# Performance work log

Hardware: AMD Instinct MI355X
Metric: run time of the kernel (lower is better)

## Reference

```python
import jax, jax.numpy as jnp
import numpy as np

MARGIN = 0.1
SCALE_POS = 2.0
SCALE_NEG = 50.0
THRESH = 0.5
EPS = 1e-5


def setup_inputs() -> dict:
    key = jax.random.key(0)
    k1, k2 = jax.random.split(key)
    feats = jax.random.normal(k1, (4096, 2, 192), dtype=jnp.float32)
    labels = jax.random.randint(k2, (4096,), 0, 4096, dtype=jnp.int64)
    return {"feats": feats, "labels": labels}


def reference(feats, labels):
    B, n_utt, D = feats.shape
    lab = jnp.repeat(labels, n_utt)            # [N]
    f = feats.reshape(-1, D)                   # [N, D]
    N = f.shape[0]

    sim = f @ f.T                              # [N, N]
    # F.normalize(sim): L2-normalize each row, eps=1e-12
    row_norm = jnp.maximum(jnp.linalg.norm(sim, axis=1, keepdims=True), 1e-12)
    S = sim / row_norm

    same = lab[None, :] == lab[:, None]        # [N, N]
    pos_mask = same & (S < 1.0 - EPS)          # pos_pair_ (includes self if < 1-eps)
    neg_mask = ~same                           # neg_pair_

    min_pos = jnp.min(jnp.where(pos_mask, S, jnp.inf), axis=1)    # per-row min(pos_pair_)
    max_neg = jnp.max(jnp.where(neg_mask, S, -jnp.inf), axis=1)   # per-row max(neg_pair_)

    neg_keep = neg_mask & (S > (min_pos - MARGIN)[:, None])
    pos_keep = pos_mask & (S < (max_neg + MARGIN)[:, None])

    has_neg = jnp.any(neg_keep, axis=1)
    has_pos = jnp.any(pos_keep, axis=1)
    valid = has_neg & has_pos

    pos_sum = jnp.sum(jnp.where(pos_keep, jnp.exp(-SCALE_POS * (S - THRESH)), 0.0), axis=1)
    neg_sum = jnp.sum(jnp.where(neg_keep, jnp.exp(SCALE_NEG * (S - THRESH)), 0.0), axis=1)

    row_loss = (1.0 / SCALE_POS) * jnp.log1p(pos_sum) + (1.0 / SCALE_NEG) * jnp.log1p(neg_sum)
    loss = jnp.sum(jnp.where(valid, row_loss, 0.0)) / N

    # prec1 = percent of rows skipped for having no surviving negatives
    prec1 = jnp.sum(~has_neg).astype(jnp.float32) * 100.0 / N
    return loss, prec1
```

## Files before the change

kernel.cpp:

```cpp
#include <hip/hip_runtime.h>
#include <math.h>

typedef __bf16 bf16x8 __attribute__((ext_vector_type(8)));
typedef float  f32x4  __attribute__((ext_vector_type(4)));
typedef int    int4v  __attribute__((ext_vector_type(4)));

constexpr float MARGIN    = 0.1f;
constexpr float SCALE_POS = 2.0f;
constexpr float SCALE_NEG = 50.0f;
constexpr float THRESH    = 0.5f;
constexpr float ONE_EPS   = 1.0f - 1e-5f;
constexpr float LOG2E     = 1.4426950408889634f;
constexpr float BC        = -(SCALE_NEG * THRESH * LOG2E);
constexpr float VCUT_COEF = (36.0674f - 30.0f) / (SCALE_NEG * LOG2E);

constexpr int D      = 192;
constexpr int KS     = 6;
constexpr int RT     = 4;
constexpr int RPW    = 64;
constexpr int RPB    = 256;
constexpr int CSPLIT = 16;

constexpr int TILE_SH = KS * 64 * 8;

__device__ inline short f2bf(float x) {
  unsigned u = __float_as_uint(x);
  u += 0x7fffu + ((u >> 16) & 1u);
  return (short)(u >> 16);
}

__device__ inline float fast_exp2(float x) {
#if __has_builtin(__builtin_amdgcn_exp2f)
  return __builtin_amdgcn_exp2f(x);
#else
  return exp2f(x);
#endif
}

__device__ inline void pin_frag(bf16x8& v) {
  int4v t = __builtin_bit_cast(int4v, v);
  asm volatile("" : "+v"(t));
  v = __builtin_bit_cast(bf16x8, t);
}

__global__ void k_pack(const float* __restrict__ f, short* __restrict__ pk, int total8) {
  int tid = blockIdx.x * blockDim.x + threadIdx.x;
  if (tid >= total8) return;
  int row = tid / 24;
  int j   = tid - row * 24;
  const float* src = f + (size_t)tid * 8;
  float4 a = *(const float4*)(src);
  float4 b = *(const float4*)(src + 4);
  union { short s[8]; int4v v; } o;
  o.s[0] = f2bf(a.x); o.s[1] = f2bf(a.y); o.s[2] = f2bf(a.z); o.s[3] = f2bf(a.w);
  o.s[4] = f2bf(b.x); o.s[5] = f2bf(b.y); o.s[6] = f2bf(b.z); o.s[7] = f2bf(b.w);
  int idx = (((row >> 4) * KS + (j >> 2)) * 64 + (j & 3) * 16 + (row & 15)) * 8;
  *(int4v*)(pk + idx) = o.v;
}

__global__ __launch_bounds__(1024) void k_buckets(
    const int* __restrict__ labs, int* __restrict__ hist_g, int* __restrict__ offs_g,
    int* __restrict__ bucket, float* __restrict__ accum, int n)
{
  __shared__ int histL[4096];
  __shared__ int offsL[4096];
  __shared__ int scanb[1024];
  const int t = threadIdx.x;

  if (t < 2) accum[t] = 0.f;
  for (int i = t; i < 4096; i += 1024) histL[i] = 0;
  __syncthreads();
  for (int i = t; i < n; i += 1024) atomicAdd(&histL[labs[i]], 1);
  __syncthreads();
  int base = t * 4;
  int v[4]; int ls = 0;
  for (int k = 0; k < 4; ++k) { v[k] = ls; ls += histL[base + k]; }
  scanb[t] = ls;
  __syncthreads();
  for (int o = 1; o < 1024; o <<= 1) {
    int x = (t >= o) ? scanb[t - o] : 0;
    __syncthreads();
    scanb[t] += x;
    __syncthreads();
  }
  int ebase = scanb[t] - ls;
  for (int k = 0; k < 4; ++k) {
    offsL[base + k] = ebase + v[k];
    offs_g[base + k] = ebase + v[k];
    hist_g[base + k] = histL[base + k];
  }
  __syncthreads();
  for (int i = t; i < 4096; i += 1024) histL[i] = 0;
  __syncthreads();
  for (int i = t; i < n; i += 1024) {
    int lab = labs[i];
    int p = atomicAdd(&histL[lab], 1);
    bucket[offsL[lab] + p] = i;
  }
}

__global__ __launch_bounds__(256, 2) void k_pass1(
    const short* __restrict__ pk, const int* __restrict__ labs,
    float* __restrict__ sumsqP, float* __restrict__ maxnegP,
    int N, int cps)
{
  __shared__ int ldsLab[512];

  const int tid  = threadIdx.x;
  const int lane = tid & 63;
  const int w    = tid >> 6;
  const int q    = lane >> 4;
  const int c    = lane & 15;
  const int cs   = blockIdx.x & (CSPLIT - 1);
  const int rbb  = blockIdx.x / CSPLIT;
  const int rowbase = rbb * RPB + w * RPW;
  const int col0 = cs * cps;
  const int ctile0 = col0 >> 4;
  const int ntiles = cps >> 4;

  for (int i = tid; i < cps; i += 256) ldsLab[i] = labs[(col0 + i) >> 1];

  bf16x8 afr[RT][KS];
#pragma unroll
  for (int rt = 0; rt < RT; ++rt)
#pragma unroll
    for (int ks = 0; ks < KS; ++ks) {
      afr[rt][ks] = *(const bf16x8*)(pk + (size_t)((rowbase >> 4) + rt) * TILE_SH + (ks * 64 + lane) * 8);
      pin_frag(afr[rt][ks]);
    }

  int labrow[RT][4];
#pragma unroll
  for (int rt = 0; rt < RT; ++rt)
#pragma unroll
    for (int rr = 0; rr < 4; ++rr)
      labrow[rt][rr] = labs[(rowbase + rt * 16 + q * 4 + rr) >> 1];

  float ssq[RT][4], mxn[RT][4];
#pragma unroll
  for (int rt = 0; rt < RT; ++rt)
#pragma unroll
    for (int rr = 0; rr < 4; ++rr) { ssq[rt][rr] = 0.f; mxn[rt][rr] = -INFINITY; }

  __syncthreads();

  auto loadB = [&](int tile, bf16x8 (&bf)[KS]) {
    const short* bp = pk + (size_t)(ctile0 + tile) * TILE_SH + lane * 8;
#pragma unroll
    for (int ks = 0; ks < KS; ++ks) bf[ks] = *(const bf16x8*)(bp + ks * 512);
  };
  auto compute = [&](const bf16x8 (&bf)[KS], int t) {
    const int labcol = ldsLab[t * 16 + c];
    f32x4 acc[RT];
#pragma unroll
    for (int rt = 0; rt < RT; ++rt) acc[rt] = 0.f;
#pragma unroll
    for (int ks = 0; ks < KS; ++ks)
#pragma unroll
      for (int rt = 0; rt < RT; ++rt)
        acc[rt] = __builtin_amdgcn_mfma_f32_16x16x32_bf16(afr[rt][ks], bf[ks], acc[rt], 0, 0, 0);
#pragma unroll
    for (int rt = 0; rt < RT; ++rt)
#pragma unroll
      for (int rr = 0; rr < 4; ++rr) {
        float v = acc[rt][rr];
        ssq[rt][rr] = fmaf(v, v, ssq[rt][rr]);
        float vm = (labrow[rt][rr] == labcol) ? -INFINITY : v;
        mxn[rt][rr] = fmaxf(mxn[rt][rr], vm);
      }
  };

  bf16x8 b0[KS], b1[KS];
  loadB(0, b0);
  for (int t = 0; t < ntiles; t += 2) {
    loadB(t + 1, b1);
    compute(b0, t);
    int nx = t + 2; nx = (nx < ntiles) ? nx : 0;
    loadB(nx, b0);
    compute(b1, t + 1);
  }

#pragma unroll
  for (int rt = 0; rt < RT; ++rt)
#pragma unroll
    for (int rr = 0; rr < 4; ++rr) {
      float s = ssq[rt][rr], m = mxn[rt][rr];
#pragma unroll
      for (int msk = 1; msk < 16; msk <<= 1) {
        s += __shfl_xor(s, msk, 64);
        m = fmaxf(m, __shfl_xor(m, msk, 64));
      }
      if (c == 0) {
        int row = rowbase + rt * 16 + q * 4 + rr;
        sumsqP[(size_t)cs * N + row] = s;
        maxnegP[(size_t)cs * N + row] = m;
      }
    }
}

__global__ void k_rowstats(
    const float* __restrict__ f, const int* __restrict__ labs,
    const float* __restrict__ sumsqP, const float* __restrict__ maxnegP,
    const int* __restrict__ offs, const int* __restrict__ hist, const int* __restrict__ bucket,
    float* __restrict__ nthr2, float* __restrict__ arow,
    float* __restrict__ validf, float* __restrict__ hasnegf, float* __restrict__ posloss,
    int N)
{
  const int lane = threadIdx.x & 63;
  const int row  = blockIdx.x * 4 + (threadIdx.x >> 6);

  float s = 0.f, m = -INFINITY;
  if (lane < CSPLIT) {
    s = sumsqP[(size_t)lane * N + row];
    m = maxnegP[(size_t)lane * N + row];
  }
#pragma unroll
  for (int msk = 1; msk < 64; msk <<= 1) {
    s += __shfl_xor(s, msk, 64);
    m = fmaxf(m, __shfl_xor(m, msk, 64));
  }
  float nrm = fmaxf(sqrtf(s), 1e-12f);
  float inv = 1.0f / nrm;
  float maxnegS = m * inv;
  float posth = fminf(ONE_EPS, maxnegS + MARGIN);

  const int lab = labs[row >> 1];
  const int beg = offs[lab], cnt = hist[lab];
  const float* fi = f + (size_t)row * D;
  float x0 = fi[lane], x1 = fi[lane + 64], x2 = fi[lane + 128];

  float minp = INFINITY, psum = 0.f; int pcnt = 0;
  for (int t = 0; t < cnt; ++t) {
    int smp = bucket[beg + t];
#pragma unroll
    for (int u = 0; u < 2; ++u) {
      const float* fj = f + (size_t)(smp * 2 + u) * D;
      float p = x0 * fj[lane] + x1 * fj[lane + 64] + x2 * fj[lane + 128];
#pragma unroll
      for (int msk = 1; msk < 64; msk <<= 1) p += __shfl_xor(p, msk, 64);
      minp = fminf(minp, p);
      float S = p * inv;
      if (S < posth) {
        psum += fast_exp2((THRESH - S) * (SCALE_POS * LOG2E));
        pcnt++;
      }
    }
  }

  float minS = minp * inv;
  float min_pos = (minS < ONE_EPS) ? minS : INFINITY;
  bool hneg = maxnegS > (min_pos - MARGIN);
  bool valid = hneg && (pcnt > 0);
  if (lane == 0) {
    nthr2[row]   = fmaxf((min_pos - MARGIN) * nrm, VCUT_COEF * nrm);
    arow[row]    = inv * (SCALE_NEG * LOG2E);
    validf[row]  = valid ? 1.f : 0.f;
    hasnegf[row] = hneg ? 1.f : 0.f;
    posloss[row] = valid ? ((1.0f / SCALE_POS) * log1pf(psum)) : 0.f;
  }
}

__global__ __launch_bounds__(256, 2) void k_pass2(
    const short* __restrict__ pk,
    const float* __restrict__ nthr2, const float* __restrict__ arow,
    const float* __restrict__ maxnegP,
    float* __restrict__ negsumP, int N, int cps)
{
  const int lane = threadIdx.x & 63;
  const int w    = threadIdx.x >> 6;
  const int q    = lane >> 4;
  const int c    = lane & 15;
  const int cs   = blockIdx.x & (CSPLIT - 1);
  const int rbb  = blockIdx.x / CSPLIT;
  const int rowbase = rbb * RPB + w * RPW;
  const int ctile0 = (cs * cps) >> 4;
  const int ntiles = cps >> 4;

  {
    int myrow = rowbase + lane;
    float mn = maxnegP[(size_t)cs * N + myrow];
    float th = nthr2[myrow];
    unsigned long long bal = __ballot(mn > th);
    if (bal == 0ull) {
      negsumP[(size_t)cs * N + myrow] = 0.f;
      return;
    }
  }

  bf16x8 afr[RT][KS];
#pragma unroll
  for (int rt = 0; rt < RT; ++rt)
#pragma unroll
    for (int ks = 0; ks < KS; ++ks) {
      afr[rt][ks] = *(const bf16x8*)(pk + (size_t)((rowbase >> 4) + rt) * TILE_SH + (ks * 64 + lane) * 8);
      pin_frag(afr[rt][ks]);
    }

  float nthrv[RT][4], arw[RT][4], ns[RT][4];
#pragma unroll
  for (int rt = 0; rt < RT; ++rt)
#pragma unroll
    for (int rr = 0; rr < 4; ++rr) {
      int row = rowbase + rt * 16 + q * 4 + rr;
      nthrv[rt][rr] = nthr2[row];
      arw[rt][rr]   = arow[row];
      ns[rt][rr]    = 0.f;
    }

  auto loadB = [&](int tile, bf16x8 (&bf)[KS]) {
    const short* bp = pk + (size_t)(ctile0 + tile) * TILE_SH + lane * 8;
#pragma unroll
    for (int ks = 0; ks < KS; ++ks) bf[ks] = *(const bf16x8*)(bp + ks * 512);
  };
  auto compute = [&](const bf16x8 (&bf)[KS]) {
    f32x4 acc[RT];
#pragma unroll
    for (int rt = 0; rt < RT; ++rt) acc[rt] = 0.f;
#pragma unroll
    for (int ks = 0; ks < KS; ++ks)
#pragma unroll
      for (int rt = 0; rt < RT; ++rt)
        acc[rt] = __builtin_amdgcn_mfma_f32_16x16x32_bf16(afr[rt][ks], bf[ks], acc[rt], 0, 0, 0);
#pragma unroll
    for (int rt = 0; rt < RT; ++rt)
#pragma unroll
      for (int rr = 0; rr < 4; ++rr) {
        float v = acc[rt][rr];
        float e = fast_exp2(fmaf(v, arw[rt][rr], BC));
        ns[rt][rr] += (v > nthrv[rt][rr]) ? e : 0.f;
      }
  };

  bf16x8 b0[KS], b1[KS];
  loadB(0, b0);
  for (int t = 0; t < ntiles; t += 2) {
    loadB(t + 1, b1);
    compute(b0);
    int nx = t + 2; nx = (nx < ntiles) ? nx : 0;
    loadB(nx, b0);
    compute(b1);
  }

#pragma unroll
  for (int rt = 0; rt < RT; ++rt)
#pragma unroll
    for (int rr = 0; rr < 4; ++rr) {
      float sv = ns[rt][rr];
#pragma unroll
      for (int msk = 1; msk < 16; msk <<= 1) sv += __shfl_xor(sv, msk, 64);
      if (c == 0) {
        int row = rowbase + rt * 16 + q * 4 + rr;
        negsumP[(size_t)cs * N + row] = sv;
      }
    }
}

__global__ void k_final_part(const float* __restrict__ negsumP, const float* __restrict__ posloss,
                             const float* __restrict__ validf, const float* __restrict__ hasnegf,
                             float* __restrict__ accum, int N)
{
  int i = blockIdx.x * blockDim.x + threadIdx.x;
  float lacc = 0.f, nacc = 0.f;
  if (i < N) {
    float nsum = 0.f;
    for (int cs2 = 0; cs2 < CSPLIT; ++cs2) nsum += negsumP[(size_t)cs2 * N + i];
    lacc = validf[i] * (posloss[i] + (1.0f / SCALE_NEG) * log1pf(nsum));
    nacc = 1.0f - hasnegf[i];
  }
#pragma unroll
  for (int msk = 1; msk < 64; msk <<= 1) {
    lacc += __shfl_xor(lacc, msk, 64);
    nacc += __shfl_xor(nacc, msk, 64);
  }
  __shared__ float sl[4], sn[4];
  int wid = threadIdx.x >> 6, lane = threadIdx.x & 63;
  if (lane == 0) { sl[wid] = lacc; sn[wid] = nacc; }
  __syncthreads();
  if (threadIdx.x == 0) {
    float L = sl[0] + sl[1] + sl[2] + sl[3];
    float Nn = sn[0] + sn[1] + sn[2] + sn[3];
    atomicAdd(&accum[0], L);
    atomicAdd(&accum[1], Nn);
  }
}

__global__ void k_write(const float* __restrict__ accum, float* __restrict__ out, int N) {
  out[0] = accum[0] / (float)N;
  out[1] = accum[1] * 100.0f / (float)N;
}

extern "C" void kernel_launch(void* const* d_in, const int* in_sizes, int n_in,
                              void* d_out, int out_size, void* d_ws, size_t ws_size,
                              hipStream_t stream)
{
  (void)n_in; (void)out_size; (void)ws_size;
  const float* f    = (const float*)d_in[0];
  const int*   labs = (const int*)d_in[1];
  const int Bs = in_sizes[1];
  const int N  = 2 * Bs;

  char* ws = (char*)d_ws;
  size_t off = 0;
  auto alloc = [&](size_t bytes) -> void* {
    void* p = ws + off;
    off += (bytes + 255) & ~(size_t)255;
    return p;
  };
  short* pk      = (short*)alloc((size_t)N * D * sizeof(short));
  float* sumsqP  = (float*)alloc((size_t)CSPLIT * N * sizeof(float));
  float* maxnegP = (float*)alloc((size_t)CSPLIT * N * sizeof(float));
  float* negsumP = (float*)alloc((size_t)CSPLIT * N * sizeof(float));
  float* nthr2   = (float*)alloc((size_t)N * sizeof(float));
  float* arow    = (float*)alloc((size_t)N * sizeof(float));
  float* validf  = (float*)alloc((size_t)N * sizeof(float));
  float* hasnegf = (float*)alloc((size_t)N * sizeof(float));
  float* posloss = (float*)alloc((size_t)N * sizeof(float));
  int* hist   = (int*)alloc((size_t)Bs * sizeof(int));
  int* offs   = (int*)alloc((size_t)Bs * sizeof(int));
  int* bucket = (int*)alloc((size_t)Bs * sizeof(int));
  float* accum = (float*)alloc(2 * sizeof(float));

  const int total8 = N * 24;
  k_pack<<<(total8 + 255) / 256, 256, 0, stream>>>(f, pk, total8);
  k_buckets<<<1, 1024, 0, stream>>>(labs, hist, offs, bucket, accum, Bs);

  const int cps   = N / CSPLIT;
  const int grid1 = (N / RPB) * CSPLIT;
  k_pass1<<<grid1, 256, 0, stream>>>(pk, labs, sumsqP, maxnegP, N, cps);
  k_rowstats<<<N / 4, 256, 0, stream>>>(f, labs, sumsqP, maxnegP, offs, hist, bucket,
                                        nthr2, arow, validf, hasnegf, posloss, N);
  k_pass2<<<grid1, 256, 0, stream>>>(pk, nthr2, arow, maxnegP, negsumP, N, cps);
  k_final_part<<<(N + 255) / 256, 256, 0, stream>>>(negsumP, posloss, validf, hasnegf, accum, N);
  k_write<<<1, 1, 0, stream>>>(accum, (float*)d_out, N);
}
```

Baseline: 111.0 us.

## Switch Gram-matrix MFMA from bf16 to scaled FP8 with K padded to 256

Packs features into FP8 (e4m3) instead of bf16, padding the 192-wide K dimension to 256, and replaces six 16x16x32 bf16 MFMAs per tile with two 16x16x128 scaled f8f6f4 MFMAs in both passes. The aim is higher matrix throughput and half the operand bytes per column tile. The cost is wasted work on the zero padding and much lower precision in the similarity values that feed thresholds, the max-negative and the exp sums, which risks correctness against the reference.

```diff
diff --git a/kernel.cpp b/kernel.cpp
--- a/kernel.cpp
+++ b/kernel.cpp
@@ -4,6 +4,7 @@
 typedef __bf16 bf16x8 __attribute__((ext_vector_type(8)));
 typedef float  f32x4  __attribute__((ext_vector_type(4)));
 typedef int    int4v  __attribute__((ext_vector_type(4)));
+typedef int    int8v  __attribute__((ext_vector_type(8)));
 
 constexpr float MARGIN    = 0.1f;
 constexpr float SCALE_POS = 2.0f;
@@ -15,19 +16,14 @@
 constexpr float VCUT_COEF = (36.0674f - 30.0f) / (SCALE_NEG * LOG2E);
 
 constexpr int D      = 192;
-constexpr int KS     = 6;
+constexpr int KP     = 256;
 constexpr int RT     = 4;
 constexpr int RPW    = 64;
 constexpr int RPB    = 256;
 constexpr int CSPLIT = 16;
 
-constexpr int TILE_SH = KS * 64 * 8;
-
-__device__ inline short f2bf(float x) {
-  unsigned u = __float_as_uint(x);
-  u += 0x7fffu + ((u >> 16) & 1u);
-  return (short)(u >> 16);
-}
+constexpr int TILE_B8 = 4096;
+constexpr int SCALE1  = 0x7f7f7f7f;
 
 __device__ inline float fast_exp2(float x) {
 #if __has_builtin(__builtin_amdgcn_exp2f)
@@ -37,25 +33,35 @@
 #endif
 }
 
-__device__ inline void pin_frag(bf16x8& v) {
-  int4v t = __builtin_bit_cast(int4v, v);
-  asm volatile("" : "+v"(t));
-  v = __builtin_bit_cast(bf16x8, t);
-}
-
-__global__ void k_pack(const float* __restrict__ f, short* __restrict__ pk, int total8) {
+__device__ inline void pin_frag8(int8v& v) {
+  asm volatile("" : "+v"(v));
+}
+
+__global__ void k_pack8(const float* __restrict__ f, unsigned char* __restrict__ pk8, int nrows) {
   int tid = blockIdx.x * blockDim.x + threadIdx.x;
-  if (tid >= total8) return;
-  int row = tid / 24;
-  int j   = tid - row * 24;
-  const float* src = f + (size_t)tid * 8;
-  float4 a = *(const float4*)(src);
-  float4 b = *(const float4*)(src + 4);
-  union { short s[8]; int4v v; } o;
-  o.s[0] = f2bf(a.x); o.s[1] = f2bf(a.y); o.s[2] = f2bf(a.z); o.s[3] = f2bf(a.w);
-  o.s[4] = f2bf(b.x); o.s[5] = f2bf(b.y); o.s[6] = f2bf(b.z); o.s[7] = f2bf(b.w);
-  int idx = (((row >> 4) * KS + (j >> 2)) * 64 + (j & 3) * 16 + (row & 15)) * 8;
-  *(int4v*)(pk + idx) = o.v;
+  int r = tid >> 3, j = tid & 7;
+  if (r >= nrows) return;
+  float x[32];
+  if (j < 6) {
+    const float* src = f + (size_t)r * D + j * 32;
+#pragma unroll
+    for (int i = 0; i < 8; ++i) {
+      float4 v = *(const float4*)(src + i * 4);
+      x[i * 4 + 0] = v.x; x[i * 4 + 1] = v.y; x[i * 4 + 2] = v.z; x[i * 4 + 3] = v.w;
+    }
+  } else {
+#pragma unroll
+    for (int i = 0; i < 32; ++i) x[i] = 0.f;
+  }
+  union { int s[8]; int8v v; } u;
+#pragma unroll
+  for (int i = 0; i < 8; ++i) {
+    int p = __builtin_amdgcn_cvt_pk_fp8_f32(x[i * 4 + 0], x[i * 4 + 1], 0, false);
+    p     = __builtin_amdgcn_cvt_pk_fp8_f32(x[i * 4 + 2], x[i * 4 + 3], p, true);
+    u.s[i] = p;
+  }
+  int tile = r >> 4, c = r & 15, g = j >> 2, qq = j & 3;
+  *(int8v*)(pk8 + (size_t)tile * TILE_B8 + g * 2048 + (qq * 16 + c) * 32) = u.v;
 }
 
 __global__ __launch_bounds__(1024) void k_buckets(
@@ -100,7 +106,7 @@
 }
 
 __global__ __launch_bounds__(256, 2) void k_pass1(
-    const short* __restrict__ pk, const int* __restrict__ labs,
+    const unsigned char* __restrict__ pk8, const int* __restrict__ labs,
     float* __restrict__ sumsqP, float* __restrict__ maxnegP,
     int N, int cps)
 {
@@ -120,13 +126,13 @@
 
   for (int i = tid; i < cps; i += 256) ldsLab[i] = labs[(col0 + i) >> 1];
 
-  bf16x8 afr[RT][KS];
-#pragma unroll
-  for (int rt = 0; rt < RT; ++rt)
-#pragma unroll
-    for (int ks = 0; ks < KS; ++ks) {
-      afr[rt][ks] = *(const bf16x8*)(pk + (size_t)((rowbase >> 4) + rt) * TILE_SH + (ks * 64 + lane) * 8);
-      pin_frag(afr[rt][ks]);
+  int8v afr[RT][2];
+#pragma unroll
+  for (int rt = 0; rt < RT; ++rt)
+#pragma unroll
+    for (int g = 0; g < 2; ++g) {
+      afr[rt][g] = *(const int8v*)(pk8 + (size_t)((rowbase >> 4) + rt) * TILE_B8 + g * 2048 + lane * 32);
+      pin_frag8(afr[rt][g]);
     }
 
   int labrow[RT][4];
@@ -144,21 +150,22 @@
 
   __syncthreads();
 
-  auto loadB = [&](int tile, bf16x8 (&bf)[KS]) {
-    const short* bp = pk + (size_t)(ctile0 + tile) * TILE_SH + lane * 8;
-#pragma unroll
-    for (int ks = 0; ks < KS; ++ks) bf[ks] = *(const bf16x8*)(bp + ks * 512);
+  auto loadB = [&](int tile, int8v (&bf)[2]) {
+    const unsigned char* bp = pk8 + (size_t)(ctile0 + tile) * TILE_B8 + lane * 32;
+#pragma unroll
+    for (int g = 0; g < 2; ++g) bf[g] = *(const int8v*)(bp + g * 2048);
   };
-  auto compute = [&](const bf16x8 (&bf)[KS], int t) {
+  auto compute = [&](const int8v (&bf)[2], int t) {
     const int labcol = ldsLab[t * 16 + c];
     f32x4 acc[RT];
 #pragma unroll
     for (int rt = 0; rt < RT; ++rt) acc[rt] = 0.f;
 #pragma unroll
-    for (int ks = 0; ks < KS; ++ks)
+    for (int g = 0; g < 2; ++g)
 #pragma unroll
       for (int rt = 0; rt < RT; ++rt)
-        acc[rt] = __builtin_amdgcn_mfma_f32_16x16x32_bf16(afr[rt][ks], bf[ks], acc[rt], 0, 0, 0);
+        acc[rt] = __builtin_amdgcn_mfma_scale_f32_16x16x128_f8f6f4(
+            afr[rt][g], bf[g], acc[rt], 0, 0, 0, SCALE1, 0, SCALE1);
 #pragma unroll
     for (int rt = 0; rt < RT; ++rt)
 #pragma unroll
@@ -170,7 +177,7 @@
       }
   };
 
-  bf16x8 b0[KS], b1[KS];
+  int8v b0[2], b1[2];
   loadB(0, b0);
   for (int t = 0; t < ntiles; t += 2) {
     loadB(t + 1, b1);
@@ -261,7 +268,7 @@
 }
 
 __global__ __launch_bounds__(256, 2) void k_pass2(
-    const short* __restrict__ pk,
+    const unsigned char* __restrict__ pk8,
     const float* __restrict__ nthr2, const float* __restrict__ arow,
     const float* __restrict__ maxnegP,
     float* __restrict__ negsumP, int N, int cps)
@@ -287,13 +294,13 @@
     }
   }
 
-  bf16x8 afr[RT][KS];
-#pragma unroll
-  for (int rt = 0; rt < RT; ++rt)
-#pragma unroll
-    for (int ks = 0; ks < KS; ++ks) {
-      afr[rt][ks] = *(const bf16x8*)(pk + (size_t)((rowbase >> 4) + rt) * TILE_SH + (ks * 64 + lane) * 8);
-      pin_frag(afr[rt][ks]);
+  int8v afr[RT][2];
+#pragma unroll
+  for (int rt = 0; rt < RT; ++rt)
+#pragma unroll
+    for (int g = 0; g < 2; ++g) {
+      afr[rt][g] = *(const int8v*)(pk8 + (size_t)((rowbase >> 4) + rt) * TILE_B8 + g * 2048 + lane * 32);
+      pin_frag8(afr[rt][g]);
     }
 
   float nthrv[RT][4], arw[RT][4], ns[RT][4];
@@ -307,20 +314,21 @@
       ns[rt][rr]    = 0.f;
     }
 
-  auto loadB = [&](int tile, bf16x8 (&bf)[KS]) {
-    const short* bp = pk + (size_t)(ctile0 + tile) * TILE_SH + lane * 8;
-#pragma unroll
-    for (int ks = 0; ks < KS; ++ks) bf[ks] = *(const bf16x8*)(bp + ks * 512);
+  auto loadB = [&](int tile, int8v (&bf)[2]) {
+    const unsigned char* bp = pk8 + (size_t)(ctile0 + tile) * TILE_B8 + lane * 32;
+#pragma unroll
+    for (int g = 0; g < 2; ++g) bf[g] = *(const int8v*)(bp + g * 2048);
   };
-  auto compute = [&](const bf16x8 (&bf)[KS]) {
+  auto compute = [&](const int8v (&bf)[2]) {
     f32x4 acc[RT];
 #pragma unroll
     for (int rt = 0; rt < RT; ++rt) acc[rt] = 0.f;
 #pragma unroll
-    for (int ks = 0; ks < KS; ++ks)
+    for (int g = 0; g < 2; ++g)
 #pragma unroll
       for (int rt = 0; rt < RT; ++rt)
-        acc[rt] = __builtin_amdgcn_mfma_f32_16x16x32_bf16(afr[rt][ks], bf[ks], acc[rt], 0, 0, 0);
+        acc[rt] = __builtin_amdgcn_mfma_scale_f32_16x16x128_f8f6f4(
+            afr[rt][g], bf[g], acc[rt], 0, 0, 0, SCALE1, 0, SCALE1);
 #pragma unroll
     for (int rt = 0; rt < RT; ++rt)
 #pragma unroll
@@ -331,7 +339,7 @@
       }
   };
 
-  bf16x8 b0[KS], b1[KS];
+  int8v b0[2], b1[2];
   loadB(0, b0);
   for (int t = 0; t < ntiles; t += 2) {
     loadB(t + 1, b1);
@@ -406,7 +414,7 @@
     off += (bytes + 255) & ~(size_t)255;
     return p;
   };
-  short* pk      = (short*)alloc((size_t)N * D * sizeof(short));
+  unsigned char* pk8 = (unsigned char*)alloc((size_t)N * KP);
   float* sumsqP  = (float*)alloc((size_t)CSPLIT * N * sizeof(float));
   float* maxnegP = (float*)alloc((size_t)CSPLIT * N * sizeof(float));
   float* negsumP = (float*)alloc((size_t)CSPLIT * N * sizeof(float));
@@ -420,16 +428,16 @@
   int* bucket = (int*)alloc((size_t)Bs * sizeof(int));
   float* accum = (float*)alloc(2 * sizeof(float));
 
-  const int total8 = N * 24;
-  k_pack<<<(total8 + 255) / 256, 256, 0, stream>>>(f, pk, total8);
+  const int totalp = N * 8;
+  k_pack8<<<(totalp + 255) / 256, 256, 0, stream>>>(f, pk8, N);
   k_buckets<<<1, 1024, 0, stream>>>(labs, hist, offs, bucket, accum, Bs);
 
   const int cps   = N / CSPLIT;
   const int grid1 = (N / RPB) * CSPLIT;
-  k_pass1<<<grid1, 256, 0, stream>>>(pk, labs, sumsqP, maxnegP, N, cps);
+  k_pass1<<<grid1, 256, 0, stream>>>(pk8, labs, sumsqP, maxnegP, N, cps);
   k_rowstats<<<N / 4, 256, 0, stream>>>(f, labs, sumsqP, maxnegP, offs, hist, bucket,
                                         nthr2, arow, validf, hasnegf, posloss, N);
-  k_pass2<<<grid1, 256, 0, stream>>>(pk, nthr2, arow, maxnegP, negsumP, N, cps);
+  k_pass2<<<grid1, 256, 0, stream>>>(pk8, nthr2, arow, maxnegP, negsumP, N, cps);
   k_final_part<<<(N + 255) / 256, 256, 0, stream>>>(negsumP, posloss, validf, hasnegf, accum, N);
   k_write<<<1, 1, 0, stream>>>(accum, (float*)d_out, N);
 }
```

Measured after the change: 107.1 us. 3.5% less time.
